# Kernel tuning notes

Measured on AMD Instinct MI355X. Metric: run time of the kernel, lower is better.

The kernel has to match this reference:

```python
import jax, jax.numpy as jnp
import numpy as np

B, L, D, CH, H = 16384, 50, 20, 16, 6


def setup_inputs() -> dict:
    key = jax.random.key(0)
    ks = jax.random.split(key, 18)
    s = 0.1
    return {
        "x": jax.random.normal(ks[0], (B, L, D), jnp.float32),
        "we_w": jax.random.normal(ks[1], (CH, D), jnp.float32) * s,
        "we_b": jax.random.normal(ks[2], (CH,), jnp.float32) * s,
        "attn_w": jax.random.normal(ks[3], (CH, CH), jnp.float32) * s,
        "attn_b": jax.random.normal(ks[4], (CH,), jnp.float32) * s,
        "conv1_w": jax.random.normal(ks[5], (CH, CH, 1), jnp.float32) * s,
        "conv1_b": jax.random.normal(ks[6], (CH,), jnp.float32) * s,
        "conv2_w": jax.random.normal(ks[7], (CH, CH, 3), jnp.float32) * s,
        "conv2_b": jax.random.normal(ks[8], (CH,), jnp.float32) * s,
        "conv3_w": jax.random.normal(ks[9], (CH, CH, 5), jnp.float32) * s,
        "conv3_b": jax.random.normal(ks[10], (CH,), jnp.float32) * s,
        "gru_wih": jax.random.normal(ks[11], (3 * H, CH), jnp.float32) * s,
        "gru_whh": jax.random.normal(ks[12], (3 * H, H), jnp.float32) * s,
        "gru_bih": jax.random.normal(ks[13], (3 * H,), jnp.float32) * s,
        "gru_bhh": jax.random.normal(ks[14], (3 * H,), jnp.float32) * s,
        "fc3_w": jax.random.normal(ks[15], (2, 3 * CH + H), jnp.float32) * s,
        "fc3_b": jax.random.normal(ks[16], (2,), jnp.float32) * s,
        "batchsize": B,
    }


def _conv1d(x, w, b, pad):
    # x: [B, C, L], w: [O, I, K] -> [B, O, L]
    y = jax.lax.conv_general_dilated(x, w, (1,), [(pad, pad)],
                                     dimension_numbers=("NCH", "OIH", "NCH"))
    return y + b[None, :, None]


def _gru(xg, wih, whh, bih, bhh):
    # xg: [B, L, CH] -> outputs [B, L, H] (PyTorch GRU equations, h0=0)
    gi = jnp.einsum("blc,gc->blg", xg, wih) + bih  # [B, L, 3H]
    gi_t = jnp.swapaxes(gi, 0, 1)                  # [L, B, 3H]
    h0 = jnp.zeros((xg.shape[0], H), xg.dtype)

    def step(h, gi_step):
        gh = h @ whh.T + bhh
        i_r, i_z, i_n = jnp.split(gi_step, 3, axis=-1)
        h_r, h_z, h_n = jnp.split(gh, 3, axis=-1)
        r = jax.nn.sigmoid(i_r + h_r)
        z = jax.nn.sigmoid(i_z + h_z)
        n = jnp.tanh(i_n + r * h_n)
        h_new = (1.0 - z) * n + z * h
        return h_new, h_new

    _, outs = jax.lax.scan(step, h0, gi_t)
    return jnp.swapaxes(outs, 0, 1)  # [B, L, H]


def reference(x, we_w, we_b, attn_w, attn_b, conv1_w, conv1_b, conv2_w, conv2_b,
              conv3_w, conv3_b, gru_wih, gru_whh, gru_bih, gru_bhh, fc3_w, fc3_b,
              batchsize):
    b = batchsize
    xe = x @ we_w.T + we_b                 # [B, L, CH]
    xr = xe.reshape(b, CH, L)              # RESHAPE (not transpose), as in torch

    lrelu = lambda v: jnp.where(v > 0, v, 0.1 * v)
    x1 = lrelu(_conv1d(xr, conv1_w, conv1_b, 0))
    x2 = lrelu(_conv1d(xr, conv2_w, conv2_b, 1))
    x3 = lrelu(_conv1d(xr, conv3_w, conv3_b, 2))

    xg = xr.reshape(b, L, CH)              # == xe
    x4 = _gru(xg, gru_wih, gru_whh, gru_bih, gru_bhh)  # [B, L, H]

    # dotproduct1: note x4.reshape([B,H,L]) is a reshape, NOT a transpose
    scores = jnp.matmul(x4, x4.reshape(b, H, L)) / H   # [B, L, L]
    alphas = jax.nn.softmax(scores, axis=1)            # softmax over dim=1 as in torch
    y = jnp.matmul(alphas, x4).reshape(b, H, L)        # [B, H, L]
    x_gru = jnp.sum(y, axis=2)                         # [B, H]

    # vectorized per-timestep attention loop: x[:, :, i] over i -> swapaxes
    xt = jnp.swapaxes(xr, 1, 2)                        # [B, L, CH]
    attn = jnp.tanh(xt @ attn_w.T + attn_b)            # [B, L, CH]
    attn1 = jnp.concatenate([attn, attn, attn], axis=2).reshape(b, 3 * CH, L)

    x_cat = jnp.concatenate([x1, x2, x3], axis=1)      # [B, 3CH, L]
    x_cnn = jnp.sum(x_cat * attn1, axis=2)             # [B, 3CH]

    feat = jnp.concatenate([x_cnn, x_gru], axis=1)     # [B, 3CH+H]
    return feat @ fc3_w.T + fc3_b                      # [B, 2]
```

## Files before the change

kernel.cpp:

```cpp
#include <hip/hip_runtime.h>

#define BATCH 16384
#define LSEQ  50
#define DIN   20
#define CHN   16
#define HID   6

typedef float vf2 __attribute__((ext_vector_type(2)));

__device__ __forceinline__ float frcp(float x){ return __builtin_amdgcn_rcpf(x); }
__device__ __forceinline__ float fsig(float x){ return frcp(1.0f + __expf(-x)); }
__device__ __forceinline__ float ftanh(float x){ float t = __expf(2.0f*x); return (t - 1.0f) * frcp(t + 1.0f); }
__device__ __forceinline__ float lrelu(float v){ return v > 0.0f ? v : 0.1f*v; }
__device__ __forceinline__ vf2 fma2(vf2 a, vf2 b, vf2 c){
#if __has_builtin(__builtin_elementwise_fma)
  return __builtin_elementwise_fma(a, b, c);
#else
  vf2 r; r.x = fmaf(a.x, b.x, c.x); r.y = fmaf(a.y, b.y, c.y); return r;
#endif
}

#define WAVE_FENCE() asm volatile("s_waitcnt lgkmcnt(0)" ::: "memory")

constexpr int SLAB = 2040;

__global__ __launch_bounds__(256, 4) void fused_kernel(
    const float* __restrict__ x,
    const float* __restrict__ we_w, const float* __restrict__ we_b,
    const float* __restrict__ attn_w, const float* __restrict__ attn_b,
    const float* __restrict__ c1w, const float* __restrict__ c1b,
    const float* __restrict__ c2w, const float* __restrict__ c2b,
    const float* __restrict__ c3w, const float* __restrict__ c3b,
    const float* __restrict__ wih, const float* __restrict__ whh,
    const float* __restrict__ bih, const float* __restrict__ bhh,
    const float* __restrict__ fc3w, const float* __restrict__ fc3b,
    float* __restrict__ out)
{
  __shared__ __align__(16) float smem[4 * SLAB];
  const int tid  = threadIdx.x;
  const int wave = tid >> 6;
  const int lane = tid & 63;
  const int b    = blockIdx.x * 4 + wave;

  float* S    = smem + wave * SLAB;
  float* sXEp = S;
  float* sY   = S;
  float* R1   = S + 840;
  float* sFE  = S + 1672;
  float* sX4  = S + 1740;

  const float* xb = x + (size_t)b * (LSEQ * DIN);

  if (lane < CHN) {
    sXEp[lane * 52]     = 0.0f;
    sXEp[lane * 52 + 1] = 0.0f;
  } else if (lane == 16) {
    sXEp[832] = 0.0f;
    sXEp[833] = 0.0f;
  }

  if (lane < LSEQ) {
    vf2 xv2[10];
    const float4* xr = (const float4*)(xb + lane * DIN);
    #pragma unroll
    for (int q = 0; q < 5; ++q) {
      float4 v = xr[q];
      vf2 p0; p0.x = v.x; p0.y = v.y;
      vf2 p1; p1.x = v.z; p1.y = v.w;
      xv2[2*q] = p0; xv2[2*q+1] = p1;
    }
    float xe[CHN];
    #pragma unroll
    for (int c = 0; c < CHN; ++c) {
      const vf2* wr = (const vf2*)(we_w + c * DIN);
      vf2 a2; a2.x = we_b[c]; a2.y = 0.0f;
      #pragma unroll
      for (int dp = 0; dp < 10; ++dp) a2 = fma2(xv2[dp], wr[dp], a2);
      xe[c] = a2.x + a2.y;
    }
    const int kk0 = lane * CHN;
    const int i0  = kk0 / 50;
    const int m0  = kk0 - i0 * 50;
    float* basep = sXEp + i0 * 52 + 2 + m0;
    #pragma unroll
    for (int c = 0; c < CHN; ++c) {
      const int off = c + ((m0 + c >= 50) ? 2 : 0);
      basep[off] = xe[c];
    }
    vf2 xe2[8];
    #pragma unroll
    for (int p = 0; p < 8; ++p) { xe2[p].x = xe[2*p]; xe2[p].y = xe[2*p+1]; }
    float gi[18];
    #pragma unroll
    for (int g = 0; g < 18; ++g) {
      const vf2* wr = (const vf2*)(wih + g * CHN);
      vf2 a2; a2.x = bih[g]; a2.y = 0.0f;
      #pragma unroll
      for (int p = 0; p < 8; ++p) a2 = fma2(xe2[p], wr[p], a2);
      gi[g] = a2.x + a2.y;
    }
    float2* gd = (float2*)(R1 + lane * 18);
    #pragma unroll
    for (int p = 0; p < 9; ++p) gd[p] = make_float2(gi[2*p], gi[2*p+1]);
  }
  __syncthreads();

  if (wave == 0) {
    const int q = lane >> 4;
    const int g = lane & 15;
    const int gb = 16 + (g & 1);
    float wa[HID], wb[HID];
    #pragma unroll
    for (int k = 0; k < HID; ++k) { wa[k] = whh[g * HID + k]; wb[k] = whh[gb * HID + k]; }
    const float ba = bhh[g];
    const float bb = bhh[gb];

    const float* giq = smem + q * SLAB + 840;
    float* x4q       = smem + q * SLAB + 1740;

    const int base = q << 4;
    const int srcZ = base + 6 + g;
    const int srcN = base + ((g < 4) ? (12 + g) : (g - 4));

    float hh[HID];
    #pragma unroll
    for (int k = 0; k < HID; ++k) hh[k] = 0.0f;

    const float* gp = giq;
    float gia = gp[g];
    float gib = gp[gb];
    for (int l = 0; l < LSEQ; ++l) {
      const float gia_c = gia;
      const float gib_c = gib;
      gp += 18;
      gia = gp[g];
      gib = gp[gb];
      float gha = ba, ghb = bb;
      #pragma unroll
      for (int k = 0; k < HID; ++k) {
        gha = fmaf(wa[k], hh[k], gha);
        ghb = fmaf(wb[k], hh[k], ghb);
      }
      const float siga = fsig(gia_c + gha);
      const float ghx = (g >= 12) ? gha : ghb;
      const float gix = (g >= 12) ? gia_c : gib_c;
      const float ghn = __shfl(ghx, srcN);
      const float gin = __shfl(gix, srcN);
      const float z   = __shfl(siga, srcZ);
      const float n   = ftanh(fmaf(siga, ghn, gin));
      const float hn  = fmaf(z, hh[g < HID ? g : 0] - n, n);
      if (g < HID) x4q[l * HID + g] = hn;
      #pragma unroll
      for (int k = 0; k < HID; ++k) hh[k] = __shfl(hn, base + k);
    }
  }
  __syncthreads();

  {
    float* sATt = R1;
    if (lane < LSEQ) {
      float a[CHN];
      #pragma unroll
      for (int cc = 0; cc < CHN; ++cc) a[cc] = sXEp[cc * 52 + 2 + lane];
      vf2 a2[8];
      #pragma unroll
      for (int p = 0; p < 8; ++p) { a2[p].x = a[2*p]; a2[p].y = a[2*p+1]; }
      #pragma unroll
      for (int c = 0; c < CHN; ++c) {
        const vf2* wr = (const vf2*)(attn_w + c * CHN);
        vf2 s2; s2.x = attn_b[c]; s2.y = 0.0f;
        #pragma unroll
        for (int p = 0; p < 8; ++p) s2 = fma2(a2[p], wr[p], s2);
        sATt[c * 52 + lane] = ftanh(s2.x + s2.y);
      }
    }
  }
  WAVE_FENCE();

  {
    const float* sATt = R1;
    const int o   = lane & 15;
    const int seg = lane >> 4;
    const int s   = seg * 12;
    const int NL  = (seg == 3) ? 14 : 12;
    vf2 Z1[7], Z2[7], Z3[7];
    #pragma unroll
    for (int p = 0; p < 7; ++p) {
      Z1[p] = (vf2)0.0f; Z2[p] = (vf2)0.0f; Z3[p] = (vf2)0.0f;
    }
    for (int i = 0; i < CHN; ++i) {
      const float w1s = c1w[o * CHN + i];
      vf2 W1; W1.x = w1s; W1.y = w1s;
      vf2 W2[3], W3[5];
      #pragma unroll
      for (int t = 0; t < 3; ++t) { float w = c2w[(o * CHN + i) * 3 + t]; W2[t].x = w; W2[t].y = w; }
      #pragma unroll
      for (int t = 0; t < 5; ++t) { float w = c3w[(o * CHN + i) * 5 + t]; W3[t].x = w; W3[t].y = w; }
      const float4* wp = (const float4*)(sXEp + i * 52 + s);
      float4 q0 = wp[0], q1 = wp[1], q2 = wp[2], q3 = wp[3], q4 = wp[4];
      float xv[20] = {q0.x,q0.y,q0.z,q0.w, q1.x,q1.y,q1.z,q1.w,
                      q2.x,q2.y,q2.z,q2.w, q3.x,q3.y,q3.z,q3.w,
                      q4.x,q4.y,q4.z,q4.w};
      vf2 XP[17];
      #pragma unroll
      for (int a = 0; a < 17; ++a) { XP[a].x = xv[a]; XP[a].y = xv[a+1]; }
      #pragma unroll
      for (int p = 0; p < 7; ++p) {
        Z1[p] = fma2(W1, XP[2*p + 2], Z1[p]);
        Z2[p] = fma2(W2[0], XP[2*p + 1], Z2[p]);
        Z2[p] = fma2(W2[1], XP[2*p + 2], Z2[p]);
        Z2[p] = fma2(W2[2], XP[2*p + 3], Z2[p]);
        Z3[p] = fma2(W3[0], XP[2*p    ], Z3[p]);
        Z3[p] = fma2(W3[1], XP[2*p + 1], Z3[p]);
        Z3[p] = fma2(W3[2], XP[2*p + 2], Z3[p]);
        Z3[p] = fma2(W3[3], XP[2*p + 3], Z3[p]);
        Z3[p] = fma2(W3[4], XP[2*p + 4], Z3[p]);
      }
    }
    const float b1v = c1b[o], b2v = c2b[o], b3v = c3b[o];
    float a1 = 0.0f, a2 = 0.0f, a3 = 0.0f;
    #pragma unroll
    for (int u = 0; u < 14; ++u) {
      if (u < NL) {
        int l = s + u;
        float v1 = lrelu(Z1[u >> 1][u & 1] + b1v);
        float v2 = lrelu(Z2[u >> 1][u & 1] + b2v);
        float v3 = lrelu(Z3[u >> 1][u & 1] + b3v);
        int f1 = o * LSEQ + l;
        int f2 = (CHN + o) * LSEQ + l;
        int f3 = (2 * CHN + o) * LSEQ + l;
        a1 += v1 * sATt[((f1 % 48) & 15) * 52 + (f1 / 48)];
        a2 += v2 * sATt[((f2 % 48) & 15) * 52 + (f2 / 48)];
        a3 += v3 * sATt[((f3 % 48) & 15) * 52 + (f3 / 48)];
      }
    }
    a1 += __shfl_xor(a1, 16); a1 += __shfl_xor(a1, 32);
    a2 += __shfl_xor(a2, 16); a2 += __shfl_xor(a2, 32);
    a3 += __shfl_xor(a3, 16); a3 += __shfl_xor(a3, 32);
    if (lane < CHN) { sFE[o] = a1; sFE[CHN + o] = a2; sFE[2 * CHN + o] = a3; }
  }
  WAVE_FENCE();

  float* sC = R1;
  if (lane < LSEQ) {
    const int xw = ((lane >> 1) & 3) << 2;
    float* rp = sC + lane * 16;
    float colj[HID];
    #pragma unroll
    for (int h = 0; h < HID; ++h) colj[h] = sX4[h * LSEQ + lane];
    vf2 cj2[3];
    #pragma unroll
    for (int p = 0; p < 3; ++p) { cj2[p].x = colj[2*p]; cj2[p].y = colj[2*p+1]; }
    *(float4*)(rp + xw)       = make_float4(colj[0], colj[1], colj[2], colj[3]);
    *(float2*)(rp + (4 ^ xw)) = make_float2(colj[4], colj[5]);
    float zs = 0.0f;
    for (int i = 0; i < LSEQ; ++i) {
      const float2 r0 = *(const float2*)(sX4 + i * 6);
      const float2 r1 = *(const float2*)(sX4 + i * 6 + 2);
      const float2 r2 = *(const float2*)(sX4 + i * 6 + 4);
      vf2 p0; p0.x = r0.x; p0.y = r0.y;
      vf2 p1; p1.x = r1.x; p1.y = r1.y;
      vf2 p2; p2.x = r2.x; p2.y = r2.y;
      vf2 s2 = (vf2)0.0f;
      s2 = fma2(p0, cj2[0], s2);
      s2 = fma2(p1, cj2[1], s2);
      s2 = fma2(p2, cj2[2], s2);
      zs += __expf((s2.x + s2.y) * (1.0f / 6.0f));
    }
    const float zi = frcp(zs);
    const float2 q0 = *(const float2*)(sX4 + lane * 6);
    const float2 q1 = *(const float2*)(sX4 + lane * 6 + 2);
    const float2 q2 = *(const float2*)(sX4 + lane * 6 + 4);
    *(float4*)(rp + (8 ^ xw))  = make_float4(zi*q0.x, zi*q0.y, zi*q1.x, zi*q1.y);
    *(float2*)(rp + (12 ^ xw)) = make_float2(zi*q2.x, zi*q2.y);
  }
  WAVE_FENCE();

  if (lane < LSEQ) {
    vf2 ri2[3];
    {
      const float2 q0 = *(const float2*)(sX4 + lane * 6);
      const float2 q1 = *(const float2*)(sX4 + lane * 6 + 2);
      const float2 q2 = *(const float2*)(sX4 + lane * 6 + 4);
      ri2[0].x = q0.x; ri2[0].y = q0.y;
      ri2[1].x = q1.x; ri2[1].y = q1.y;
      ri2[2].x = q2.x; ri2[2].y = q2.y;
    }
    vf2 ya2[3];
    #pragma unroll
    for (int p = 0; p < 3; ++p) ya2[p] = (vf2)0.0f;
    auto acc_row = [&](const float* rp, const int xw) {
      const float4 t0 = *(const float4*)(rp + xw);
      const float2 t1 = *(const float2*)(rp + (4 ^ xw));
      vf2 p0; p0.x = t0.x; p0.y = t0.y;
      vf2 p1; p1.x = t0.z; p1.y = t0.w;
      vf2 p2; p2.x = t1.x; p2.y = t1.y;
      vf2 s2 = (vf2)0.0f;
      s2 = fma2(ri2[0], p0, s2);
      s2 = fma2(ri2[1], p1, s2);
      s2 = fma2(ri2[2], p2, s2);
      const float e = __expf((s2.x + s2.y) * (1.0f / 6.0f));
      vf2 e2; e2.x = e; e2.y = e;
      const float4 w0 = *(const float4*)(rp + (8 ^ xw));
      const float2 w1 = *(const float2*)(rp + (12 ^ xw));
      vf2 wv0; wv0.x = w0.x; wv0.y = w0.y;
      vf2 wv1; wv1.x = w0.z; wv1.y = w0.w;
      vf2 wv2; wv2.x = w1.x; wv2.y = w1.y;
      ya2[0] = fma2(e2, wv0, ya2[0]);
      ya2[1] = fma2(e2, wv1, ya2[1]);
      ya2[2] = fma2(e2, wv2, ya2[2]);
    };
    for (int jb = 0; jb < 48; jb += 8) {
      const float* cp = sC + jb * 16;
      #pragma unroll
      for (int d = 0; d < 8; ++d) acc_row(cp + d * 16, ((d >> 1) & 3) << 2);
    }
    acc_row(sC + 48 * 16, 0);
    acc_row(sC + 49 * 16, 0);
    *(float2*)(sY + lane * 6)     = make_float2(ya2[0].x, ya2[0].y);
    *(float2*)(sY + lane * 6 + 2) = make_float2(ya2[1].x, ya2[1].y);
    *(float2*)(sY + lane * 6 + 4) = make_float2(ya2[2].x, ya2[2].y);
  }
  WAVE_FENCE();

  if (lane < 48) {
    const int h = lane >> 3;
    const int m = lane & 7;
    float s = 0.0f;
    #pragma unroll
    for (int k = 0; k < 7; ++k) {
      const int idx = m + (k << 3);
      if (idx < LSEQ) s += sY[h * LSEQ + idx];
    }
    s += __shfl_xor(s, 1);
    s += __shfl_xor(s, 2);
    s += __shfl_xor(s, 4);
    if (m == 0) sFE[48 + h] = s;
  }
  WAVE_FENCE();

  {
    const int oo = lane & 1;
    const int kk = lane >> 1;
    float s = fc3w[oo * 54 + kk] * sFE[kk];
    if (kk < 22) s = fmaf(fc3w[oo * 54 + kk + 32], sFE[kk + 32], s);
    s += __shfl_xor(s, 2);
    s += __shfl_xor(s, 4);
    s += __shfl_xor(s, 8);
    s += __shfl_xor(s, 16);
    s += __shfl_xor(s, 32);
    if (lane < 2) out[(size_t)b * 2 + lane] = s + fc3b[lane];
  }
}

extern "C" void kernel_launch(void* const* d_in, const int* in_sizes, int n_in,
                              void* d_out, int out_size, void* d_ws, size_t ws_size,
                              hipStream_t stream) {
  (void)in_sizes; (void)n_in; (void)d_ws; (void)ws_size; (void)out_size;
  fused_kernel<<<BATCH / 4, 256, 0, stream>>>(
      (const float*)d_in[0],
      (const float*)d_in[1],  (const float*)d_in[2],
      (const float*)d_in[3],  (const float*)d_in[4],
      (const float*)d_in[5],  (const float*)d_in[6],
      (const float*)d_in[7],  (const float*)d_in[8],
      (const float*)d_in[9],  (const float*)d_in[10],
      (const float*)d_in[11], (const float*)d_in[12],
      (const float*)d_in[13], (const float*)d_in[14],
      (const float*)d_in[15], (const float*)d_in[16],
      (float*)d_out);
}
```

Before: 284.0 us.

## Run GRU recurrence per wave instead of wave 0 serving four slabs

Moves the GRU recurrence from wave 0 handling four sequences in 16-lane groups (bracketed by block-wide barriers) to each wave running its own sequence on 16 lanes with only wave-local fences. The hidden state is broadcast through LDS reads rather than six shuffles, and the recurrent dot products use packed FMA. Exponentials become direct exp2 with folded log2e constants, and the softmax denominator loop is unrolled with two accumulators, keeping the row operands in registers. This removes the serialization of the recurrence onto one wave and the block barriers, but adds an LDS round trip on each recurrent step.

```diff
diff --git a/kernel.cpp b/kernel.cpp
--- a/kernel.cpp
+++ b/kernel.cpp
@@ -9,8 +9,16 @@
 typedef float vf2 __attribute__((ext_vector_type(2)));
 
 __device__ __forceinline__ float frcp(float x){ return __builtin_amdgcn_rcpf(x); }
-__device__ __forceinline__ float fsig(float x){ return frcp(1.0f + __expf(-x)); }
-__device__ __forceinline__ float ftanh(float x){ float t = __expf(2.0f*x); return (t - 1.0f) * frcp(t + 1.0f); }
+__device__ __forceinline__ float fexp2(float x){
+#if __has_builtin(__builtin_amdgcn_exp2f)
+  return __builtin_amdgcn_exp2f(x);
+#else
+  return exp2f(x);
+#endif
+}
+#define LOG2E 1.4426950408889634f
+__device__ __forceinline__ float fsig(float x){ return frcp(1.0f + fexp2(-LOG2E * x)); }
+__device__ __forceinline__ float ftanh(float x){ float t = fexp2((2.0f*LOG2E)*x); return (t - 1.0f) * frcp(t + 1.0f); }
 __device__ __forceinline__ float lrelu(float v){ return v > 0.0f ? v : 0.1f*v; }
 __device__ __forceinline__ vf2 fma2(vf2 a, vf2 b, vf2 c){
 #if __has_builtin(__builtin_elementwise_fma)
@@ -19,6 +27,7 @@
   vf2 r; r.x = fmaf(a.x, b.x, c.x); r.y = fmaf(a.y, b.y, c.y); return r;
 #endif
 }
+#define KEXP 0.24044917348149793f
 
 #define WAVE_FENCE() asm volatile("s_waitcnt lgkmcnt(0)" ::: "memory")
 
@@ -103,58 +112,62 @@
     #pragma unroll
     for (int p = 0; p < 9; ++p) gd[p] = make_float2(gi[2*p], gi[2*p+1]);
   }
-  __syncthreads();
-
-  if (wave == 0) {
-    const int q = lane >> 4;
-    const int g = lane & 15;
+  WAVE_FENCE();
+
+  if (lane < 16) {
+    const int g  = lane;
     const int gb = 16 + (g & 1);
-    float wa[HID], wb[HID];
-    #pragma unroll
-    for (int k = 0; k < HID; ++k) { wa[k] = whh[g * HID + k]; wb[k] = whh[gb * HID + k]; }
+    vf2 wa2[3], wb2[3];
+    #pragma unroll
+    for (int k = 0; k < 3; ++k) {
+      const float2 a = *(const float2*)(whh + g  * HID + 2*k);
+      const float2 c = *(const float2*)(whh + gb * HID + 2*k);
+      wa2[k].x = a.x; wa2[k].y = a.y;
+      wb2[k].x = c.x; wb2[k].y = c.y;
+    }
     const float ba = bhh[g];
     const float bb = bhh[gb];
-
-    const float* giq = smem + q * SLAB + 840;
-    float* x4q       = smem + q * SLAB + 1740;
-
-    const int base = q << 4;
-    const int srcZ = base + 6 + g;
-    const int srcN = base + ((g < 4) ? (12 + g) : (g - 4));
-
-    float hh[HID];
-    #pragma unroll
-    for (int k = 0; k < HID; ++k) hh[k] = 0.0f;
-
-    const float* gp = giq;
-    float gia = gp[g];
-    float gib = gp[gb];
+    const int srcZ = 6 + g;
+    const int srcN = (g < 4) ? (12 + g) : (g - 4);
+
+    vf2 hh2[3];
+    #pragma unroll
+    for (int k = 0; k < 3; ++k) hh2[k] = (vf2)0.0f;
+    float hprev = 0.0f;
+
+    const float* gp = R1;
     for (int l = 0; l < LSEQ; ++l) {
-      const float gia_c = gia;
-      const float gib_c = gib;
+      const float gia = gp[g];
+      const float gib = gp[gb];
       gp += 18;
-      gia = gp[g];
-      gib = gp[gb];
-      float gha = ba, ghb = bb;
-      #pragma unroll
-      for (int k = 0; k < HID; ++k) {
-        gha = fmaf(wa[k], hh[k], gha);
-        ghb = fmaf(wb[k], hh[k], ghb);
+      vf2 aa; aa.x = ba; aa.y = 0.0f;
+      vf2 ab; ab.x = bb; ab.y = 0.0f;
+      #pragma unroll
+      for (int k = 0; k < 3; ++k) {
+        aa = fma2(wa2[k], hh2[k], aa);
+        ab = fma2(wb2[k], hh2[k], ab);
       }
-      const float siga = fsig(gia_c + gha);
+      const float gha = aa.x + aa.y;
+      const float ghb = ab.x + ab.y;
+      const float siga = fsig(gia + gha);
       const float ghx = (g >= 12) ? gha : ghb;
-      const float gix = (g >= 12) ? gia_c : gib_c;
+      const float gix = (g >= 12) ? gia : gib;
       const float ghn = __shfl(ghx, srcN);
       const float gin = __shfl(gix, srcN);
       const float z   = __shfl(siga, srcZ);
       const float n   = ftanh(fmaf(siga, ghn, gin));
-      const float hn  = fmaf(z, hh[g < HID ? g : 0] - n, n);
-      if (g < HID) x4q[l * HID + g] = hn;
-      #pragma unroll
-      for (int k = 0; k < HID; ++k) hh[k] = __shfl(hn, base + k);
-    }
-  }
-  __syncthreads();
+      const float hn  = fmaf(z, hprev - n, n);
+      hprev = hn;
+      if (g < HID) sX4[l * HID + g] = hn;
+      const float2 h01 = *(const float2*)(sX4 + l * HID);
+      const float2 h23 = *(const float2*)(sX4 + l * HID + 2);
+      const float2 h45 = *(const float2*)(sX4 + l * HID + 4);
+      hh2[0].x = h01.x; hh2[0].y = h01.y;
+      hh2[1].x = h23.x; hh2[1].y = h23.y;
+      hh2[2].x = h45.x; hh2[2].y = h45.y;
+    }
+  }
+  WAVE_FENCE();
 
   {
     float* sATt = R1;
@@ -242,6 +255,7 @@
   WAVE_FENCE();
 
   float* sC = R1;
+  vf2 ri2[3];
   if (lane < LSEQ) {
     const int xw = ((lane >> 1) & 3) << 2;
     float* rp = sC + lane * 16;
@@ -253,39 +267,45 @@
     for (int p = 0; p < 3; ++p) { cj2[p].x = colj[2*p]; cj2[p].y = colj[2*p+1]; }
     *(float4*)(rp + xw)       = make_float4(colj[0], colj[1], colj[2], colj[3]);
     *(float2*)(rp + (4 ^ xw)) = make_float2(colj[4], colj[5]);
-    float zs = 0.0f;
-    for (int i = 0; i < LSEQ; ++i) {
+    float zs0 = 0.0f, zs1 = 0.0f;
+    #pragma unroll
+    for (int i = 0; i < LSEQ; i += 2) {
       const float2 r0 = *(const float2*)(sX4 + i * 6);
       const float2 r1 = *(const float2*)(sX4 + i * 6 + 2);
       const float2 r2 = *(const float2*)(sX4 + i * 6 + 4);
+      vf2 s2 = (vf2)0.0f;
       vf2 p0; p0.x = r0.x; p0.y = r0.y;
       vf2 p1; p1.x = r1.x; p1.y = r1.y;
       vf2 p2; p2.x = r2.x; p2.y = r2.y;
-      vf2 s2 = (vf2)0.0f;
       s2 = fma2(p0, cj2[0], s2);
       s2 = fma2(p1, cj2[1], s2);
       s2 = fma2(p2, cj2[2], s2);
-      zs += __expf((s2.x + s2.y) * (1.0f / 6.0f));
-    }
-    const float zi = frcp(zs);
+      zs0 += fexp2((s2.x + s2.y) * KEXP);
+      const float2 t0 = *(const float2*)(sX4 + (i + 1) * 6);
+      const float2 t1 = *(const float2*)(sX4 + (i + 1) * 6 + 2);
+      const float2 t2 = *(const float2*)(sX4 + (i + 1) * 6 + 4);
+      vf2 u2 = (vf2)0.0f;
+      vf2 v0; v0.x = t0.x; v0.y = t0.y;
+      vf2 v1; v1.x = t1.x; v1.y = t1.y;
+      vf2 v2; v2.x = t2.x; v2.y = t2.y;
+      u2 = fma2(v0, cj2[0], u2);
+      u2 = fma2(v1, cj2[1], u2);
+      u2 = fma2(v2, cj2[2], u2);
+      zs1 += fexp2((u2.x + u2.y) * KEXP);
+    }
+    const float zi = frcp(zs0 + zs1);
     const float2 q0 = *(const float2*)(sX4 + lane * 6);
     const float2 q1 = *(const float2*)(sX4 + lane * 6 + 2);
     const float2 q2 = *(const float2*)(sX4 + lane * 6 + 4);
+    ri2[0].x = q0.x; ri2[0].y = q0.y;
+    ri2[1].x = q1.x; ri2[1].y = q1.y;
+    ri2[2].x = q2.x; ri2[2].y = q2.y;
     *(float4*)(rp + (8 ^ xw))  = make_float4(zi*q0.x, zi*q0.y, zi*q1.x, zi*q1.y);
     *(float2*)(rp + (12 ^ xw)) = make_float2(zi*q2.x, zi*q2.y);
   }
   WAVE_FENCE();
 
   if (lane < LSEQ) {
-    vf2 ri2[3];
-    {
-      const float2 q0 = *(const float2*)(sX4 + lane * 6);
-      const float2 q1 = *(const float2*)(sX4 + lane * 6 + 2);
-      const float2 q2 = *(const float2*)(sX4 + lane * 6 + 4);
-      ri2[0].x = q0.x; ri2[0].y = q0.y;
-      ri2[1].x = q1.x; ri2[1].y = q1.y;
-      ri2[2].x = q2.x; ri2[2].y = q2.y;
-    }
     vf2 ya2[3];
     #pragma unroll
     for (int p = 0; p < 3; ++p) ya2[p] = (vf2)0.0f;
@@ -299,7 +319,7 @@
       s2 = fma2(ri2[0], p0, s2);
       s2 = fma2(ri2[1], p1, s2);
       s2 = fma2(ri2[2], p2, s2);
-      const float e = __expf((s2.x + s2.y) * (1.0f / 6.0f));
+      const float e = fexp2((s2.x + s2.y) * KEXP);
       vf2 e2; e2.x = e; e2.y = e;
       const float4 w0 = *(const float4*)(rp + (8 ^ xw));
       const float2 w1 = *(const float2*)(rp + (12 ^ xw));
```

Result: faster. 276.5 us (-2.6%).
